# Performance work log

Measured on AMD Instinct MI355X. Metric: run time of the kernel, lower is better.

## Reference

```python
import jax, jax.numpy as jnp
import numpy as np

IN_FEATURES = 1_000_000
OUT_FEATURE_SETS = 4
NUM_CHUNKS = 2500
SPLIT_SIZE = 400  # ceil(IN_FEATURES / NUM_CHUNKS); padding = 0 here
BATCH = 64


def setup_inputs() -> dict:
    key = jax.random.key(0)
    k1, k2, k3 = jax.random.split(key, 3)
    x = jax.random.normal(k1, (BATCH, IN_FEATURES), dtype=jnp.float32)
    weight = jax.random.normal(k2, (OUT_FEATURE_SETS, SPLIT_SIZE, NUM_CHUNKS), dtype=jnp.float32)
    bias = jax.random.normal(k3, (OUT_FEATURE_SETS * NUM_CHUNKS,), dtype=jnp.float32)
    return {"x": x, "weight": weight, "bias": bias}


def reference(x, weight, bias):
    # weight: [O, S, C]
    O, S, C = weight.shape
    B = x.shape[0]
    pad = S * C - x.shape[1]
    if pad > 0:
        x = jnp.pad(x, ((0, 0), (0, pad)))
    xr = x.reshape(B, S, C)  # [B, S, C]
    # per set o: sum over split dim S, keep chunk dim C -> [B, O, C]
    out = jnp.einsum('bsc,osc->boc', xr, weight)
    # torch cat over sets along dim=1 => set-major flatten [B, O*C]
    return out.reshape(B, O * C) + bias
```

## Files before the change

### kernel.cpp

```cpp
#include <hip/hip_runtime.h>


constexpr int IN_F   = 1000000;
constexpr int S_DIM  = 400;
constexpr int C_DIM  = 2500;
constexpr int O_SETS = 4;
constexpr int B_SZ   = 64;
constexpr int OC     = O_SETS * C_DIM;
constexpr int OUT_N  = B_SZ * OC;

constexpr int NQ     = C_DIM / 4;
constexpr int QW     = (NQ + 63) / 64;
constexpr int NSPLIT = 16;
constexpr int SSEG   = S_DIM / NSPLIT;
constexpr int STEPQ  = C_DIM / 4;

constexpr size_t WS_NEED = (size_t)NSPLIT * OUT_N * sizeof(float);

__device__ __forceinline__ void fma4(float4& a, const float4& p, const float4& q) {
    a.x = fmaf(p.x, q.x, a.x);
    a.y = fmaf(p.y, q.y, a.y);
    a.z = fmaf(p.z, q.z, a.z);
    a.w = fmaf(p.w, q.w, a.w);
}


__global__ __launch_bounds__(64) void sl_part(const float* __restrict__ x,
                                              const float* __restrict__ w,
                                              float* __restrict__ ws) {
    const int lane = threadIdx.x;
    const int q    = blockIdx.x * 64 + lane;
    if (q >= NQ) return;
    const int b  = blockIdx.y;
    const int z  = blockIdx.z;
    const int s0 = z * SSEG;

    const float4* xp = (const float4*)(x + (size_t)b * IN_F + (size_t)s0 * C_DIM) + q;
    const float4* wp[O_SETS];
#pragma unroll
    for (int o = 0; o < O_SETS; ++o)
        wp[o] = (const float4*)(w + (size_t)o * (S_DIM * C_DIM) + (size_t)s0 * C_DIM) + q;

    float4 acc[O_SETS];
#pragma unroll
    for (int o = 0; o < O_SETS; ++o) acc[o] = make_float4(0.f, 0.f, 0.f, 0.f);

    float4 xb[2], wb[2][O_SETS];
    xb[0] = *xp; xp += STEPQ;
#pragma unroll
    for (int o = 0; o < O_SETS; ++o) { wb[0][o] = *wp[o]; wp[o] += STEPQ; }

#pragma unroll
    for (int s = 0; s < SSEG; ++s) {
        const int cur = s & 1, nxt = cur ^ 1;
        if (s + 1 < SSEG) {
            xb[nxt] = *xp; xp += STEPQ;
#pragma unroll
            for (int o = 0; o < O_SETS; ++o) { wb[nxt][o] = *wp[o]; wp[o] += STEPQ; }
        }
#pragma unroll
        for (int o = 0; o < O_SETS; ++o)
            fma4(acc[o], xb[cur], wb[cur][o]);
    }

    float* orow = ws + (size_t)z * OUT_N + (size_t)b * OC;
#pragma unroll
    for (int o = 0; o < O_SETS; ++o)
        *(float4*)(orow + o * C_DIM + q * 4) = acc[o];
}

__global__ __launch_bounds__(256) void sl_reduce(const float* __restrict__ ws,
                                                 const float* __restrict__ bias,
                                                 float* __restrict__ out) {
    const int t = blockIdx.x * 256 + threadIdx.x;
    if (t >= OUT_N / 4) return;
    const int idx = t * 4;
    const int oc  = idx % OC;

    float4 s = *(const float4*)(bias + oc);
#pragma unroll
    for (int z = 0; z < NSPLIT; ++z) {
        float4 v = *(const float4*)(ws + (size_t)z * OUT_N + idx);
        s.x += v.x; s.y += v.y; s.z += v.z; s.w += v.w;
    }
    *(float4*)(out + idx) = s;
}


__global__ __launch_bounds__(256) void sl_init(const float* __restrict__ bias,
                                               float* __restrict__ out) {
    int j = blockIdx.x * 256 + threadIdx.x;
    if (j < OC) out[(size_t)blockIdx.y * OC + j] = bias[j];
}

__global__ __launch_bounds__(64) void sl_atomic(const float* __restrict__ x,
                                                const float* __restrict__ w,
                                                float* __restrict__ out) {
    const int lane = threadIdx.x;
    const int q    = blockIdx.x * 64 + lane;
    if (q >= NQ) return;
    const int b  = blockIdx.y;
    const int s0 = blockIdx.z * SSEG;

    const float4* xp = (const float4*)(x + (size_t)b * IN_F + (size_t)s0 * C_DIM) + q;
    const float4* wp[O_SETS];
#pragma unroll
    for (int o = 0; o < O_SETS; ++o)
        wp[o] = (const float4*)(w + (size_t)o * (S_DIM * C_DIM) + (size_t)s0 * C_DIM) + q;

    float4 acc[O_SETS];
#pragma unroll
    for (int o = 0; o < O_SETS; ++o) acc[o] = make_float4(0.f, 0.f, 0.f, 0.f);

    for (int s = 0; s < SSEG; ++s) {
        float4 xv = *xp; xp += STEPQ;
        float4 wv[O_SETS];
#pragma unroll
        for (int o = 0; o < O_SETS; ++o) { wv[o] = *wp[o]; wp[o] += STEPQ; }
#pragma unroll
        for (int o = 0; o < O_SETS; ++o) fma4(acc[o], xv, wv[o]);
    }

    float* orow = out + (size_t)b * OC;
#pragma unroll
    for (int o = 0; o < O_SETS; ++o) {
        float* dst = orow + o * C_DIM + q * 4;
        atomicAdd(dst + 0, acc[o].x);
        atomicAdd(dst + 1, acc[o].y);
        atomicAdd(dst + 2, acc[o].z);
        atomicAdd(dst + 3, acc[o].w);
    }
}

extern "C" void kernel_launch(void* const* d_in, const int* in_sizes, int n_in,
                              void* d_out, int out_size, void* d_ws, size_t ws_size,
                              hipStream_t stream) {
    const float* x    = (const float*)d_in[0];
    const float* wgt  = (const float*)d_in[1];
    const float* bias = (const float*)d_in[2];
    float* out = (float*)d_out;

    if (ws_size >= WS_NEED) {
        float* ws = (float*)d_ws;
        dim3 g(QW, B_SZ, NSPLIT);
        sl_part<<<g, 64, 0, stream>>>(x, wgt, ws);
        sl_reduce<<<(OUT_N / 4 + 255) / 256, 256, 0, stream>>>(ws, bias, out);
    } else {
        dim3 gInit((OC + 255) / 256, B_SZ);
        sl_init<<<gInit, 256, 0, stream>>>(bias, out);
        dim3 g(QW, B_SZ, NSPLIT);
        sl_atomic<<<g, 64, 0, stream>>>(x, wgt, out);
    }
}
```

Baseline: 399.6 us.

## Stage weight tiles in LDS and reuse across batch rows per block

The split-K partial kernel now loads a 4x16x64 float4 weight tile into shared memory once per block. Each of four waves reuses it for 8 batch rows, processed as two passes of 4 rows with register accumulators. Before, every batch row re-read the full weight slab from global memory, so this cuts weight traffic by about 32x. The split count rises from 16 to 25 so each segment covers 16 rows of S. That enlarges the workspace and the reduce work and raises register pressure from the 16 float4 accumulators.

Result: slower. 437.1 us (+9.4%).

```diff
diff --git a/kernel.cpp b/kernel.cpp
--- a/kernel.cpp
+++ b/kernel.cpp
@@ -11,9 +11,11 @@
 
 constexpr int NQ     = C_DIM / 4;
 constexpr int QW     = (NQ + 63) / 64;
-constexpr int NSPLIT = 16;
+constexpr int NSPLIT = 25;
 constexpr int SSEG   = S_DIM / NSPLIT;
-constexpr int STEPQ  = C_DIM / 4;
+constexpr int BG     = 2;
+constexpr int BPW    = 8;
+constexpr int BT_IN  = 4;
 
 constexpr size_t WS_NEED = (size_t)NSPLIT * OUT_N * sizeof(float);
 
@@ -25,48 +27,85 @@
 }
 
 
-__global__ __launch_bounds__(64) void sl_part(const float* __restrict__ x,
-                                              const float* __restrict__ w,
-                                              float* __restrict__ ws) {
-    const int lane = threadIdx.x;
-    const int q    = blockIdx.x * 64 + lane;
-    if (q >= NQ) return;
-    const int b  = blockIdx.y;
-    const int z  = blockIdx.z;
-    const int s0 = z * SSEG;
+__global__ __launch_bounds__(256) void sl_part(const float* __restrict__ x,
+                                               const float* __restrict__ w,
+                                               float* __restrict__ ws) {
+    __shared__ float4 wlds[O_SETS][SSEG][64];
 
-    const float4* xp = (const float4*)(x + (size_t)b * IN_F + (size_t)s0 * C_DIM) + q;
-    const float4* wp[O_SETS];
-#pragma unroll
-    for (int o = 0; o < O_SETS; ++o)
-        wp[o] = (const float4*)(w + (size_t)o * (S_DIM * C_DIM) + (size_t)s0 * C_DIM) + q;
-
-    float4 acc[O_SETS];
-#pragma unroll
-    for (int o = 0; o < O_SETS; ++o) acc[o] = make_float4(0.f, 0.f, 0.f, 0.f);
-
-    float4 xb[2], wb[2][O_SETS];
-    xb[0] = *xp; xp += STEPQ;
-#pragma unroll
-    for (int o = 0; o < O_SETS; ++o) { wb[0][o] = *wp[o]; wp[o] += STEPQ; }
+    const int tid = threadIdx.x;
+    const int q0  = blockIdx.x * 64;
+    const int z   = blockIdx.z;
+    const int s0  = z * SSEG;
 
 #pragma unroll
-    for (int s = 0; s < SSEG; ++s) {
-        const int cur = s & 1, nxt = cur ^ 1;
-        if (s + 1 < SSEG) {
-            xb[nxt] = *xp; xp += STEPQ;
+    for (int k = 0; k < 16; ++k) {
+        const int f   = tid + k * 256;
+        const int r   = f >> 6;
+        const int col = f & 63;
+        const int o   = r >> 4;
+        const int s   = r & 15;
+        int gq = q0 + col; if (gq >= NQ) gq = NQ - 1;
+        wlds[o][s][col] =
+            *(const float4*)(w + (size_t)o * (S_DIM * C_DIM)
+                               + (size_t)(s0 + s) * C_DIM + (size_t)gq * 4);
+    }
+    __syncthreads();
+
+    const int lane = tid & 63;
+    const int wv   = tid >> 6;
+    const int q    = q0 + lane;
+    const bool act = (q < NQ);
+    const int qc   = act ? q : 0;
+
 #pragma unroll
-            for (int o = 0; o < O_SETS; ++o) { wb[nxt][o] = *wp[o]; wp[o] += STEPQ; }
+    for (int pass = 0; pass < 2; ++pass) {
+        const int b0 = blockIdx.y * (BPW * 4) + wv * BPW + pass * BT_IN;
+
+        const float4* xp[BT_IN];
+#pragma unroll
+        for (int i = 0; i < BT_IN; ++i)
+            xp[i] = (const float4*)(x + (size_t)(b0 + i) * IN_F
+                                      + (size_t)s0 * C_DIM) + qc;
+
+        float4 acc[BT_IN][O_SETS];
+#pragma unroll
+        for (int i = 0; i < BT_IN; ++i)
+#pragma unroll
+            for (int o = 0; o < O_SETS; ++o)
+                acc[i][o] = make_float4(0.f, 0.f, 0.f, 0.f);
+
+        float4 xb[2][BT_IN];
+#pragma unroll
+        for (int i = 0; i < BT_IN; ++i) { xb[0][i] = *xp[i]; xp[i] += C_DIM / 4; }
+
+#pragma unroll
+        for (int s = 0; s < SSEG; ++s) {
+            const int cur = s & 1, nxt = cur ^ 1;
+            if (s + 1 < SSEG) {
+#pragma unroll
+                for (int i = 0; i < BT_IN; ++i) { xb[nxt][i] = *xp[i]; xp[i] += C_DIM / 4; }
+            }
+            float4 wv4[O_SETS];
+#pragma unroll
+            for (int o = 0; o < O_SETS; ++o) wv4[o] = wlds[o][s][lane];
+#pragma unroll
+            for (int i = 0; i < BT_IN; ++i)
+#pragma unroll
+                for (int o = 0; o < O_SETS; ++o)
+                    fma4(acc[i][o], xb[cur][i], wv4[o]);
         }
+
+        if (act) {
+            float* base = ws + (size_t)z * OUT_N;
 #pragma unroll
-        for (int o = 0; o < O_SETS; ++o)
-            fma4(acc[o], xb[cur], wb[cur][o]);
+            for (int i = 0; i < BT_IN; ++i) {
+                float* orow = base + (size_t)(b0 + i) * OC;
+#pragma unroll
+                for (int o = 0; o < O_SETS; ++o)
+                    *(float4*)(orow + o * C_DIM + q * 4) = acc[i][o];
+            }
+        }
     }
-
-    float* orow = ws + (size_t)z * OUT_N + (size_t)b * OC;
-#pragma unroll
-    for (int o = 0; o < O_SETS; ++o)
-        *(float4*)(orow + o * C_DIM + q * 4) = acc[o];
 }
 
 __global__ __launch_bounds__(256) void sl_reduce(const float* __restrict__ ws,
@@ -113,12 +152,12 @@
     for (int o = 0; o < O_SETS; ++o) acc[o] = make_float4(0.f, 0.f, 0.f, 0.f);
 
     for (int s = 0; s < SSEG; ++s) {
-        float4 xv = *xp; xp += STEPQ;
-        float4 wv[O_SETS];
+        float4 xv = *xp; xp += C_DIM / 4;
+        float4 wv4[O_SETS];
 #pragma unroll
-        for (int o = 0; o < O_SETS; ++o) { wv[o] = *wp[o]; wp[o] += STEPQ; }
+        for (int o = 0; o < O_SETS; ++o) { wv4[o] = *wp[o]; wp[o] += C_DIM / 4; }
 #pragma unroll
-        for (int o = 0; o < O_SETS; ++o) fma4(acc[o], xv, wv[o]);
+        for (int o = 0; o < O_SETS; ++o) fma4(acc[o], xv, wv4[o]);
     }
 
     float* orow = out + (size_t)b * OC;
@@ -142,8 +181,8 @@
 
     if (ws_size >= WS_NEED) {
         float* ws = (float*)d_ws;
-        dim3 g(QW, B_SZ, NSPLIT);
-        sl_part<<<g, 64, 0, stream>>>(x, wgt, ws);
+        dim3 g(QW, BG, NSPLIT);
+        sl_part<<<g, 256, 0, stream>>>(x, wgt, ws);
         sl_reduce<<<(OUT_N / 4 + 255) / 256, 256, 0, stream>>>(ws, bias, out);
     } else {
         dim3 gInit((OC + 255) / 256, B_SZ);
```

## Hold weight segment in registers and reuse across batch groups

Applied to the files above, without the earlier changes.

The partial-sum kernel now loads each thread's weight slice for its S-segment into registers once. It then loops over 16 batch rows, double-buffering the x loads, so weights are no longer re-read for every batch row. The S split goes from 16 to 50 so the register-held weight slice stays small. This makes the workspace and the reduce pass much larger, and a smaller workspace would push execution onto the atomic fallback. The grid also becomes much smaller, which lowers latency hiding. The reduce kernel gets two independent accumulators to shorten its dependency chain.

Measured after the change: 399.9 us. About the same (+0.1%).

```diff
diff --git a/kernel.cpp b/kernel.cpp
--- a/kernel.cpp
+++ b/kernel.cpp
@@ -11,9 +11,10 @@
 
 constexpr int NQ     = C_DIM / 4;
 constexpr int QW     = (NQ + 63) / 64;
-constexpr int NSPLIT = 16;
+constexpr int NSPLIT = 50;
 constexpr int SSEG   = S_DIM / NSPLIT;
-constexpr int STEPQ  = C_DIM / 4;
+constexpr int BPW    = 16;
+constexpr int BGRP   = B_SZ / BPW;
 
 constexpr size_t WS_NEED = (size_t)NSPLIT * OUT_N * sizeof(float);
 
@@ -25,48 +26,75 @@
 }
 
 
-__global__ __launch_bounds__(64) void sl_part(const float* __restrict__ x,
-                                              const float* __restrict__ w,
-                                              float* __restrict__ ws) {
+__global__ __launch_bounds__(64, 2) void sl_part(const float* __restrict__ x,
+                                                 const float* __restrict__ w,
+                                                 float* __restrict__ ws) {
     const int lane = threadIdx.x;
     const int q    = blockIdx.x * 64 + lane;
-    if (q >= NQ) return;
-    const int b  = blockIdx.y;
-    const int z  = blockIdx.z;
-    const int s0 = z * SSEG;
+    const bool act = (q < NQ);
+    const int qc   = act ? q : NQ - 1;
+    const int b0   = blockIdx.y * BPW;
+    const int z    = blockIdx.z;
+    const int s0   = z * SSEG;
 
-    const float4* xp = (const float4*)(x + (size_t)b * IN_F + (size_t)s0 * C_DIM) + q;
-    const float4* wp[O_SETS];
+    float4 wreg[O_SETS][SSEG];
 #pragma unroll
     for (int o = 0; o < O_SETS; ++o)
-        wp[o] = (const float4*)(w + (size_t)o * (S_DIM * C_DIM) + (size_t)s0 * C_DIM) + q;
+#pragma unroll
+        for (int s = 0; s < SSEG; ++s)
+            wreg[o][s] = *(const float4*)(w + (size_t)o * (S_DIM * C_DIM)
+                                            + (size_t)(s0 + s) * C_DIM
+                                            + (size_t)qc * 4);
 
+    const float* xbase = x + (size_t)s0 * C_DIM + (size_t)qc * 4;
+
+    float4 xb[2][4];
     float4 acc[O_SETS];
 #pragma unroll
     for (int o = 0; o < O_SETS; ++o) acc[o] = make_float4(0.f, 0.f, 0.f, 0.f);
 
-    float4 xb[2], wb[2][O_SETS];
-    xb[0] = *xp; xp += STEPQ;
+    {
+        const float* row = xbase + (size_t)b0 * IN_F;
 #pragma unroll
-    for (int o = 0; o < O_SETS; ++o) { wb[0][o] = *wp[o]; wp[o] += STEPQ; }
+        for (int j = 0; j < 4; ++j)
+            xb[0][j] = *(const float4*)(row + (size_t)j * C_DIM);
+    }
+
+    for (int b = 0; b < BPW; ++b) {
+        const float* row = xbase + (size_t)(b0 + b) * IN_F;
 
 #pragma unroll
-    for (int s = 0; s < SSEG; ++s) {
-        const int cur = s & 1, nxt = cur ^ 1;
-        if (s + 1 < SSEG) {
-            xb[nxt] = *xp; xp += STEPQ;
+        for (int j = 0; j < 4; ++j)
+            xb[1][j] = *(const float4*)(row + (size_t)(4 + j) * C_DIM);
+
 #pragma unroll
-            for (int o = 0; o < O_SETS; ++o) { wb[nxt][o] = *wp[o]; wp[o] += STEPQ; }
+        for (int j = 0; j < 4; ++j)
+#pragma unroll
+            for (int o = 0; o < O_SETS; ++o)
+                fma4(acc[o], xb[0][j], wreg[o][j]);
+
+        if (b + 1 < BPW) {
+            const float* nrow = xbase + (size_t)(b0 + b + 1) * IN_F;
+#pragma unroll
+            for (int j = 0; j < 4; ++j)
+                xb[0][j] = *(const float4*)(nrow + (size_t)j * C_DIM);
+        }
+
+#pragma unroll
+        for (int j = 0; j < 4; ++j)
+#pragma unroll
+            for (int o = 0; o < O_SETS; ++o)
+                fma4(acc[o], xb[1][j], wreg[o][4 + j]);
+
+        if (act) {
+            float* orow = ws + (size_t)z * OUT_N + (size_t)(b0 + b) * OC;
+#pragma unroll
+            for (int o = 0; o < O_SETS; ++o)
+                *(float4*)(orow + o * C_DIM + q * 4) = acc[o];
         }
 #pragma unroll
-        for (int o = 0; o < O_SETS; ++o)
-            fma4(acc[o], xb[cur], wb[cur][o]);
+        for (int o = 0; o < O_SETS; ++o) acc[o] = make_float4(0.f, 0.f, 0.f, 0.f);
     }
-
-    float* orow = ws + (size_t)z * OUT_N + (size_t)b * OC;
-#pragma unroll
-    for (int o = 0; o < O_SETS; ++o)
-        *(float4*)(orow + o * C_DIM + q * 4) = acc[o];
 }
 
 __global__ __launch_bounds__(256) void sl_reduce(const float* __restrict__ ws,
@@ -77,13 +105,17 @@
     const int idx = t * 4;
     const int oc  = idx % OC;
 
-    float4 s = *(const float4*)(bias + oc);
-#pragma unroll
-    for (int z = 0; z < NSPLIT; ++z) {
-        float4 v = *(const float4*)(ws + (size_t)z * OUT_N + idx);
-        s.x += v.x; s.y += v.y; s.z += v.z; s.w += v.w;
+    float4 s0 = *(const float4*)(bias + oc);
+    float4 s1 = make_float4(0.f, 0.f, 0.f, 0.f);
+#pragma unroll 10
+    for (int z = 0; z < NSPLIT; z += 2) {
+        float4 v0 = *(const float4*)(ws + (size_t)z * OUT_N + idx);
+        float4 v1 = *(const float4*)(ws + (size_t)(z + 1) * OUT_N + idx);
+        s0.x += v0.x; s0.y += v0.y; s0.z += v0.z; s0.w += v0.w;
+        s1.x += v1.x; s1.y += v1.y; s1.z += v1.z; s1.w += v1.w;
     }
-    *(float4*)(out + idx) = s;
+    s0.x += s1.x; s0.y += s1.y; s0.z += s1.z; s0.w += s1.w;
+    *(float4*)(out + idx) = s0;
 }
 
 
@@ -113,12 +145,12 @@
     for (int o = 0; o < O_SETS; ++o) acc[o] = make_float4(0.f, 0.f, 0.f, 0.f);
 
     for (int s = 0; s < SSEG; ++s) {
-        float4 xv = *xp; xp += STEPQ;
-        float4 wv[O_SETS];
+        float4 xv = *xp; xp += C_DIM / 4;
+        float4 wv4[O_SETS];
 #pragma unroll
-        for (int o = 0; o < O_SETS; ++o) { wv[o] = *wp[o]; wp[o] += STEPQ; }
+        for (int o = 0; o < O_SETS; ++o) { wv4[o] = *wp[o]; wp[o] += C_DIM / 4; }
 #pragma unroll
-        for (int o = 0; o < O_SETS; ++o) fma4(acc[o], xv, wv[o]);
+        for (int o = 0; o < O_SETS; ++o) fma4(acc[o], xv, wv4[o]);
     }
 
     float* orow = out + (size_t)b * OC;
@@ -142,7 +174,7 @@
 
     if (ws_size >= WS_NEED) {
         float* ws = (float*)d_ws;
-        dim3 g(QW, B_SZ, NSPLIT);
+        dim3 g(QW, BGRP, NSPLIT);
         sl_part<<<g, 64, 0, stream>>>(x, wgt, ws);
         sl_reduce<<<(OUT_N / 4 + 255) / 256, 256, 0, stream>>>(ws, bias, out);
     } else {
```

## Register-tile four batch rows per thread to reuse weight loads

Applied to the files above, without the earlier changes.

The partial-sum kernel now has each 256-thread block process four batch rows at once, so every weight float4 loaded is reused across four x rows instead of being re-fetched per batch row. The grid shrinks accordingly and out-of-range lanes are clamped instead of exiting early. The reduction kernel splits its sum into two independent accumulators for more load-level parallelism. The cost is higher register use per thread and some idle lanes in the last column block.

Measured after the change: 377.0 us. -5.7%, faster.

```diff
diff --git a/kernel.cpp b/kernel.cpp
--- a/kernel.cpp
+++ b/kernel.cpp
@@ -10,9 +10,11 @@
 constexpr int OUT_N  = B_SZ * OC;
 
 constexpr int NQ     = C_DIM / 4;
-constexpr int QW     = (NQ + 63) / 64;
+constexpr int CB     = 3;
 constexpr int NSPLIT = 16;
 constexpr int SSEG   = S_DIM / NSPLIT;
+constexpr int BT     = 4;
+constexpr int BGRP   = B_SZ / BT;
 constexpr int STEPQ  = C_DIM / 4;
 
 constexpr size_t WS_NEED = (size_t)NSPLIT * OUT_N * sizeof(float);
@@ -25,28 +27,37 @@
 }
 
 
-__global__ __launch_bounds__(64) void sl_part(const float* __restrict__ x,
-                                              const float* __restrict__ w,
-                                              float* __restrict__ ws) {
-    const int lane = threadIdx.x;
-    const int q    = blockIdx.x * 64 + lane;
-    if (q >= NQ) return;
-    const int b  = blockIdx.y;
-    const int z  = blockIdx.z;
-    const int s0 = z * SSEG;
+__global__ __launch_bounds__(256, 2) void sl_part(const float* __restrict__ x,
+                                                  const float* __restrict__ w,
+                                                  float* __restrict__ ws) {
+    const int tid = threadIdx.x;
+    const int q   = blockIdx.x * 256 + tid;
+    const bool act = (q < NQ);
+    const int qc  = act ? q : NQ - 1;
+    const int b0  = blockIdx.y * BT;
+    const int z   = blockIdx.z;
+    const int s0  = z * SSEG;
 
-    const float4* xp = (const float4*)(x + (size_t)b * IN_F + (size_t)s0 * C_DIM) + q;
+    const float4* xp[BT];
+#pragma unroll
+    for (int i = 0; i < BT; ++i)
+        xp[i] = (const float4*)(x + (size_t)(b0 + i) * IN_F + (size_t)s0 * C_DIM) + qc;
+
     const float4* wp[O_SETS];
 #pragma unroll
     for (int o = 0; o < O_SETS; ++o)
-        wp[o] = (const float4*)(w + (size_t)o * (S_DIM * C_DIM) + (size_t)s0 * C_DIM) + q;
+        wp[o] = (const float4*)(w + (size_t)o * (S_DIM * C_DIM) + (size_t)s0 * C_DIM) + qc;
 
-    float4 acc[O_SETS];
+    float4 acc[BT][O_SETS];
 #pragma unroll
-    for (int o = 0; o < O_SETS; ++o) acc[o] = make_float4(0.f, 0.f, 0.f, 0.f);
+    for (int i = 0; i < BT; ++i)
+#pragma unroll
+        for (int o = 0; o < O_SETS; ++o)
+            acc[i][o] = make_float4(0.f, 0.f, 0.f, 0.f);
 
-    float4 xb[2], wb[2][O_SETS];
-    xb[0] = *xp; xp += STEPQ;
+    float4 xb[2][BT], wb[2][O_SETS];
+#pragma unroll
+    for (int i = 0; i < BT; ++i) { xb[0][i] = *xp[i]; xp[i] += STEPQ; }
 #pragma unroll
     for (int o = 0; o < O_SETS; ++o) { wb[0][o] = *wp[o]; wp[o] += STEPQ; }
 
@@ -54,19 +65,28 @@
     for (int s = 0; s < SSEG; ++s) {
         const int cur = s & 1, nxt = cur ^ 1;
         if (s + 1 < SSEG) {
-            xb[nxt] = *xp; xp += STEPQ;
+#pragma unroll
+            for (int i = 0; i < BT; ++i) { xb[nxt][i] = *xp[i]; xp[i] += STEPQ; }
 #pragma unroll
             for (int o = 0; o < O_SETS; ++o) { wb[nxt][o] = *wp[o]; wp[o] += STEPQ; }
         }
 #pragma unroll
-        for (int o = 0; o < O_SETS; ++o)
-            fma4(acc[o], xb[cur], wb[cur][o]);
+        for (int i = 0; i < BT; ++i)
+#pragma unroll
+            for (int o = 0; o < O_SETS; ++o)
+                fma4(acc[i][o], xb[cur][i], wb[cur][o]);
     }
 
-    float* orow = ws + (size_t)z * OUT_N + (size_t)b * OC;
+    if (act) {
+        float* base = ws + (size_t)z * OUT_N;
 #pragma unroll
-    for (int o = 0; o < O_SETS; ++o)
-        *(float4*)(orow + o * C_DIM + q * 4) = acc[o];
+        for (int i = 0; i < BT; ++i) {
+            float* orow = base + (size_t)(b0 + i) * OC;
+#pragma unroll
+            for (int o = 0; o < O_SETS; ++o)
+                *(float4*)(orow + o * C_DIM + q * 4) = acc[i][o];
+        }
+    }
 }
 
 __global__ __launch_bounds__(256) void sl_reduce(const float* __restrict__ ws,
@@ -77,13 +97,17 @@
     const int idx = t * 4;
     const int oc  = idx % OC;
 
-    float4 s = *(const float4*)(bias + oc);
+    float4 s0 = *(const float4*)(bias + oc);
+    float4 s1 = make_float4(0.f, 0.f, 0.f, 0.f);
 #pragma unroll
-    for (int z = 0; z < NSPLIT; ++z) {
-        float4 v = *(const float4*)(ws + (size_t)z * OUT_N + idx);
-        s.x += v.x; s.y += v.y; s.z += v.z; s.w += v.w;
+    for (int z = 0; z < NSPLIT; z += 2) {
+        float4 v0 = *(const float4*)(ws + (size_t)z * OUT_N + idx);
+        float4 v1 = *(const float4*)(ws + (size_t)(z + 1) * OUT_N + idx);
+        s0.x += v0.x; s0.y += v0.y; s0.z += v0.z; s0.w += v0.w;
+        s1.x += v1.x; s1.y += v1.y; s1.z += v1.z; s1.w += v1.w;
     }
-    *(float4*)(out + idx) = s;
+    s0.x += s1.x; s0.y += s1.y; s0.z += s1.z; s0.w += s1.w;
+    *(float4*)(out + idx) = s0;
 }
 
 
@@ -114,11 +138,11 @@
 
     for (int s = 0; s < SSEG; ++s) {
         float4 xv = *xp; xp += STEPQ;
-        float4 wv[O_SETS];
+        float4 wv4[O_SETS];
 #pragma unroll
-        for (int o = 0; o < O_SETS; ++o) { wv[o] = *wp[o]; wp[o] += STEPQ; }
+        for (int o = 0; o < O_SETS; ++o) { wv4[o] = *wp[o]; wp[o] += STEPQ; }
 #pragma unroll
-        for (int o = 0; o < O_SETS; ++o) fma4(acc[o], xv, wv[o]);
+        for (int o = 0; o < O_SETS; ++o) fma4(acc[o], xv, wv4[o]);
     }
 
     float* orow = out + (size_t)b * OC;
@@ -142,13 +166,13 @@
 
     if (ws_size >= WS_NEED) {
         float* ws = (float*)d_ws;
-        dim3 g(QW, B_SZ, NSPLIT);
-        sl_part<<<g, 64, 0, stream>>>(x, wgt, ws);
+        dim3 g(CB, BGRP, NSPLIT);
+        sl_part<<<g, 256, 0, stream>>>(x, wgt, ws);
         sl_reduce<<<(OUT_N / 4 + 255) / 256, 256, 0, stream>>>(ws, bias, out);
     } else {
         dim3 gInit((OC + 255) / 256, B_SZ);
         sl_init<<<gInit, 256, 0, stream>>>(bias, out);
-        dim3 g(QW, B_SZ, NSPLIT);
+        dim3 g((NQ + 63) / 64, B_SZ, NSPLIT);
         sl_atomic<<<g, 64, 0, stream>>>(x, wgt, out);
     }
 }
```
